# Kernel optimization log

Hardware: AMD Instinct MI355X
Metric: run time of the kernel (lower is better)

## Reference

```python
import jax, jax.numpy as jnp
import numpy as np

SEQ, D_IN, D_OUT = 8192, 768, 128


def setup_inputs() -> dict:
    key = jax.random.key(0)
    k1, k2, k3, k4 = jax.random.split(key, 4)
    x = jax.random.normal(k1, (SEQ, D_IN), dtype=jnp.float32)
    # torch nn.Linear weights are stored as [d_out, d_in]
    scale = 1.0 / np.sqrt(D_IN)
    w_query = jax.random.normal(k2, (D_OUT, D_IN), dtype=jnp.float32) * scale
    w_key = jax.random.normal(k3, (D_OUT, D_IN), dtype=jnp.float32) * scale
    w_value = jax.random.normal(k4, (D_OUT, D_IN), dtype=jnp.float32) * scale
    return {"x": x, "w_query": w_query, "w_key": w_key, "w_value": w_value}


def reference(x, w_query, w_key, w_value):
    # Linear with bias=False: y = x @ W.T   (W is [d_out, d_in])
    q = x @ w_query.T                      # [N, d_out]
    k = x @ w_key.T                        # [N, d_out]
    v = x @ w_value.T                      # [N, d_out]
    inv_sqrt_d = 1.0 / jnp.sqrt(jnp.float32(k.shape[-1]))
    scores = (q @ k.T) * inv_sqrt_d        # [N, N] -- fully materialized, as in source
    weights = jax.nn.softmax(scores, axis=-1)
    return weights @ v                     # [N, d_out]
```

## Files before the change

### kernel.cpp

```cpp
#include <hip/hip_runtime.h>
#include <stdint.h>

#define SEQ 8192
#define DIN 768
#define DOUT 128

typedef __attribute__((ext_vector_type(8))) short short8;
typedef __attribute__((ext_vector_type(8))) unsigned short ushort8v;
typedef __attribute__((ext_vector_type(4))) float f32x4;

#define CEXPF (1.4426950408889634f * 0.08838834764831845f)

#if __has_builtin(__builtin_amdgcn_exp2f)
#define EXP2(x) __builtin_amdgcn_exp2f(x)
#else
#define EXP2(x) __builtin_exp2f(x)
#endif

__device__ __forceinline__ unsigned short f2bf(float f) {
  return (unsigned short)((__float_as_uint(f) + 0x8000u) >> 16);
}

__device__ __forceinline__ void gload_lds16(const void* g, void* l) {
  __builtin_amdgcn_global_load_lds(
      (const __attribute__((address_space(1))) void*)g,
      (__attribute__((address_space(3))) void*)l, 16, 0, 0);
}

__global__ void wconv_kernel(const float* __restrict__ wq,
                             const float* __restrict__ wk,
                             const float* __restrict__ wv,
                             unsigned short* __restrict__ Wb) {
  int idx4 = (blockIdx.x * 256 + threadIdx.x) * 4;
  int z = idx4 / (DOUT * DIN);
  int rem = idx4 - z * (DOUT * DIN);
  const float* src = (z == 0) ? wq : (z == 1) ? wk : wv;
  float4 v = *(const float4*)(src + rem);
  float sc = (z == 0) ? CEXPF : 1.0f;
  ushort4 o;
  o.x = f2bf(v.x * sc); o.y = f2bf(v.y * sc);
  o.z = f2bf(v.z * sc); o.w = f2bf(v.w * sc);
  *(ushort4*)(Wb + idx4) = o;
}

__launch_bounds__(256, 3)
__global__ void qkv_kernel(const float* __restrict__ x,
                           const unsigned short* __restrict__ Wb,
                           unsigned short* __restrict__ Qb,
                           unsigned short* __restrict__ Kb,
                           unsigned short* __restrict__ Vtb) {
  __shared__ unsigned short smem[4352];
  unsigned short* xs = smem;

  const int t    = threadIdx.x;
  const int w    = t >> 6;
  const int lane = t & 63;
  const int g    = lane >> 4;
  const int r    = lane & 15;
  const int z    = blockIdx.y;
  const int m0   = blockIdx.x * 32;
  const unsigned short* Wz = Wb + (size_t)z * DOUT * DIN;

  f32x4 acc[2][2];
#pragma unroll
  for (int i = 0; i < 2; i++)
#pragma unroll
    for (int j = 0; j < 2; j++) acc[i][j] = 0.f;

  const int srow = t >> 3;
  const int scol = (t & 7) * 4;

#pragma unroll 1
  for (int kb = 0; kb < DIN; kb += 32) {
    short8 af[2];
#pragma unroll
    for (int mt = 0; mt < 2; mt++)
      af[mt] = *(const short8*)(Wz + (size_t)(w * 32 + mt * 16 + r) * DIN + kb + g * 8);
    float4 xv = *(const float4*)(x + (size_t)(m0 + srow) * DIN + kb + scol);
    ushort4 xb;
    xb.x = f2bf(xv.x); xb.y = f2bf(xv.y); xb.z = f2bf(xv.z); xb.w = f2bf(xv.w);
    *(ushort4*)&xs[srow * 40 + scol] = xb;
    __syncthreads();
    short8 bf[2];
#pragma unroll
    for (int nt = 0; nt < 2; nt++)
      bf[nt] = *(const short8*)&xs[(nt * 16 + r) * 40 + g * 8];
#pragma unroll
    for (int mt = 0; mt < 2; mt++)
#pragma unroll
      for (int nt = 0; nt < 2; nt++)
        acc[mt][nt] = __builtin_amdgcn_mfma_f32_16x16x32_bf16(af[mt], bf[nt], acc[mt][nt], 0, 0, 0);
    __syncthreads();
  }

  if (z < 2) {
    unsigned short* out = (z == 0) ? Qb : Kb;
#pragma unroll
    for (int mt = 0; mt < 2; mt++)
#pragma unroll
      for (int nt = 0; nt < 2; nt++) {
        ushort4 o;
        o.x = f2bf(acc[mt][nt][0]); o.y = f2bf(acc[mt][nt][1]);
        o.z = f2bf(acc[mt][nt][2]); o.w = f2bf(acc[mt][nt][3]);
        *(ushort4*)(out + (size_t)(m0 + nt * 16 + r) * DOUT + w * 32 + mt * 16 + g * 4) = o;
      }
  } else {
    unsigned short* ct = smem;
#pragma unroll
    for (int mt = 0; mt < 2; mt++)
#pragma unroll
      for (int nt = 0; nt < 2; nt++) {
        ushort4 o;
        o.x = f2bf(acc[mt][nt][0]); o.y = f2bf(acc[mt][nt][1]);
        o.z = f2bf(acc[mt][nt][2]); o.w = f2bf(acc[mt][nt][3]);
        *(ushort4*)&ct[(nt * 16 + r) * 136 + w * 32 + mt * 16 + g * 4] = o;
      }
    __syncthreads();
    int col  = t >> 1;
    int half = (t & 1) * 16;
#pragma unroll
    for (int h2 = 0; h2 < 2; h2++) {
      ushort8v a;
#pragma unroll
      for (int i = 0; i < 8; i++) a[i] = ct[(half + h2 * 8 + i) * 136 + col];
      *(ushort8v*)(Vtb + (size_t)col * SEQ + m0 + half + h2 * 8) = a;
    }
  }
}

__launch_bounds__(256, 2)
__global__ void attn_kernel(const unsigned short* __restrict__ Qb,
                            const unsigned short* __restrict__ Kb,
                            const unsigned short* __restrict__ Vtb,
                            float* __restrict__ Opart,
                            float* __restrict__ lpart) {
  __shared__ unsigned char lds[51200];
  unsigned char* Kl = lds;
  unsigned char* Vl = lds + 16384;

  const int t    = threadIdx.x;
  const int wave = t >> 6;
  const int lane = t & 63;
  const int g    = lane >> 4;
  const int r    = lane & 15;
  unsigned short* Pl = (unsigned short*)(lds + 32768 + wave * 4608);

  const int qb = blockIdx.x;
  const int sp = blockIdx.y;
  const int q0 = qb * 128 + wave * 32;

  short8 qf[2][4];
#pragma unroll
  for (int nt = 0; nt < 2; nt++)
#pragma unroll
    for (int kc = 0; kc < 4; kc++)
      qf[nt][kc] = *(const short8*)(Qb + (size_t)(q0 + nt * 16 + r) * DOUT + kc * 32 + g * 8);

  short8 onesf;
#pragma unroll
  for (int j = 0; j < 8; j++) onesf[j] = (r == 0) ? (short)0x3F80 : (short)0;

  f32x4 oacc[2][8];
  f32x4 lacc[2];
#pragma unroll
  for (int st = 0; st < 2; st++) {
    lacc[st] = 0.f;
#pragma unroll
    for (int n = 0; n < 8; n++) oacc[st][n] = 0.f;
  }

#pragma unroll 1
  for (int it = 0; it < 16; it++) {
    const int kv0 = sp * 1024 + it * 64;
#pragma unroll
    for (int c = 0; c < 4; c++) {
      int idx = (wave * 4 + c) * 64 + lane;
      int krow = idx >> 4, kch = idx & 15;
      gload_lds16(Kb + ((size_t)(kv0 + krow) << 7) + ((kch ^ (krow & 15)) << 3),
                  Kl + ((wave * 4 + c) << 10) + (lane << 4));
      int d = idx >> 3, c2 = idx & 7;
      gload_lds16(Vtb + (size_t)d * SEQ + kv0 + ((c2 ^ (d & 7)) << 3),
                  Vl + ((wave * 4 + c) << 10) + (lane << 4));
    }
    __syncthreads();

    f32x4 sf[4][2];
#pragma unroll
    for (int mt = 0; mt < 4; mt++)
#pragma unroll
      for (int nt = 0; nt < 2; nt++) sf[mt][nt] = 0.f;
#pragma unroll
    for (int mt = 0; mt < 4; mt++) {
      int row = mt * 16 + r;
#pragma unroll
      for (int kc = 0; kc < 4; kc++) {
        short8 kf = *(const short8*)(Kl + row * 256 + (((kc * 4 + g) ^ (row & 15)) << 4));
        sf[mt][0] = __builtin_amdgcn_mfma_f32_16x16x32_bf16(kf, qf[0][kc], sf[mt][0], 0, 0, 0);
        sf[mt][1] = __builtin_amdgcn_mfma_f32_16x16x32_bf16(kf, qf[1][kc], sf[mt][1], 0, 0, 0);
      }
    }

#pragma unroll
    for (int mt = 0; mt < 4; mt++)
#pragma unroll
      for (int nt = 0; nt < 2; nt++) {
        ushort4 p;
        p.x = f2bf(EXP2(sf[mt][nt][0]));
        p.y = f2bf(EXP2(sf[mt][nt][1]));
        p.z = f2bf(EXP2(sf[mt][nt][2]));
        p.w = f2bf(EXP2(sf[mt][nt][3]));
        *(ushort4*)(Pl + (nt * 16 + r) * 72 + mt * 16 + g * 4) = p;
      }
    short8 pf[2][2];
#pragma unroll
    for (int st = 0; st < 2; st++)
#pragma unroll
      for (int c2 = 0; c2 < 2; c2++)
        pf[st][c2] = *(const short8*)(Pl + (st * 16 + r) * 72 + c2 * 32 + g * 8);

#pragma unroll
    for (int nt = 0; nt < 8; nt++) {
      int d = nt * 16 + r;
#pragma unroll
      for (int c2 = 0; c2 < 2; c2++) {
        short8 vf = *(const short8*)(Vl + d * 128 + (((c2 * 4 + g) ^ (d & 7)) << 4));
        oacc[0][nt] = __builtin_amdgcn_mfma_f32_16x16x32_bf16(pf[0][c2], vf, oacc[0][nt], 0, 0, 0);
        oacc[1][nt] = __builtin_amdgcn_mfma_f32_16x16x32_bf16(pf[1][c2], vf, oacc[1][nt], 0, 0, 0);
      }
    }
#pragma unroll
    for (int st = 0; st < 2; st++) {
      lacc[st] = __builtin_amdgcn_mfma_f32_16x16x32_bf16(pf[st][0], onesf, lacc[st], 0, 0, 0);
      lacc[st] = __builtin_amdgcn_mfma_f32_16x16x32_bf16(pf[st][1], onesf, lacc[st], 0, 0, 0);
    }
    __syncthreads();
  }

  const size_t pbase = (size_t)sp * SEQ;
#pragma unroll
  for (int st = 0; st < 2; st++)
#pragma unroll
    for (int rr = 0; rr < 4; rr++) {
      int qrow = q0 + st * 16 + g * 4 + rr;
#pragma unroll
      for (int nt = 0; nt < 8; nt++)
        Opart[(pbase + qrow) * DOUT + nt * 16 + r] = oacc[st][nt][rr];
      if (r == 0) lpart[pbase + qrow] = lacc[st][rr];
    }
}

__global__ void combine_kernel(const float* __restrict__ Opart,
                               const float* __restrict__ lpart,
                               float* __restrict__ out) {
  int idx = blockIdx.x * 256 + threadIdx.x;
  int s   = idx >> 5;
  int d4  = (idx & 31) * 4;
  float L = 0.f;
  f32x4 acc = 0.f;
#pragma unroll
  for (int p = 0; p < 8; p++) {
    L += lpart[p * SEQ + s];
    acc += *(const f32x4*)(Opart + ((size_t)p * SEQ + s) * DOUT + d4);
  }
  f32x4 res = acc * (1.0f / L);
  *(f32x4*)(out + (size_t)s * DOUT + d4) = res;
}

extern "C" void kernel_launch(void* const* d_in, const int* in_sizes, int n_in,
                              void* d_out, int out_size, void* d_ws, size_t ws_size,
                              hipStream_t stream) {
  const float* x  = (const float*)d_in[0];
  const float* wq = (const float*)d_in[1];
  const float* wk = (const float*)d_in[2];
  const float* wv = (const float*)d_in[3];
  float* out = (float*)d_out;

  unsigned short* Qb  = (unsigned short*)d_ws;
  unsigned short* Kb  = Qb + (size_t)SEQ * DOUT;
  unsigned short* Vtb = Kb + (size_t)SEQ * DOUT;
  float* Opart = (float*)(Vtb + (size_t)SEQ * DOUT);
  float* lpart = Opart + (size_t)8 * SEQ * DOUT;
  unsigned short* Wb  = (unsigned short*)Opart;
  if (ws_size < (size_t)(6291456 + 33554432 + 262144)) return;

  wconv_kernel<<<dim3(288), 256, 0, stream>>>(wq, wk, wv, Wb);
  qkv_kernel<<<dim3(256, 3), 256, 0, stream>>>(x, Wb, Qb, Kb, Vtb);
  attn_kernel<<<dim3(64, 8), 256, 0, stream>>>(Qb, Kb, Vtb, Opart, lpart);
  combine_kernel<<<dim3(1024), 256, 0, stream>>>(Opart, lpart, out);
}
```

Before: 136.4 us.

## Pre-convert x to bf16 and retile QKV projection with async LDS loads

The separate weight-conversion kernel now also converts x to bf16 up front. The QKV projection uses 128-row tiles with a K step of 64, and stages both x and W into XOR-swizzled LDS through global_load_lds. This is meant to raise data reuse per block and cut redundant global W reads in the projection stage. The cost is an extra full pass over x plus a bf16 copy in workspace, and only 192 blocks, which may underfill the GPU.

```diff
diff --git a/kernel.cpp b/kernel.cpp
--- a/kernel.cpp
+++ b/kernel.cpp
@@ -27,30 +27,45 @@
       (__attribute__((address_space(3))) void*)l, 16, 0, 0);
 }
 
-__global__ void wconv_kernel(const float* __restrict__ wq,
-                             const float* __restrict__ wk,
-                             const float* __restrict__ wv,
-                             unsigned short* __restrict__ Wb) {
+#define XELEMS (SEQ * DIN)
+#define WELEMS (DOUT * DIN)
+__global__ void conv_kernel(const float* __restrict__ x,
+                            const float* __restrict__ wq,
+                            const float* __restrict__ wk,
+                            const float* __restrict__ wv,
+                            unsigned short* __restrict__ xb,
+                            unsigned short* __restrict__ Wb) {
   int idx4 = (blockIdx.x * 256 + threadIdx.x) * 4;
-  int z = idx4 / (DOUT * DIN);
-  int rem = idx4 - z * (DOUT * DIN);
-  const float* src = (z == 0) ? wq : (z == 1) ? wk : wv;
-  float4 v = *(const float4*)(src + rem);
-  float sc = (z == 0) ? CEXPF : 1.0f;
+  const float* src;
+  unsigned short* dst;
+  float sc = 1.0f;
+  if (idx4 < XELEMS) {
+    src = x + idx4;
+    dst = xb + idx4;
+  } else {
+    int wi = idx4 - XELEMS;
+    int z  = wi / WELEMS;
+    int rem = wi - z * WELEMS;
+    src = ((z == 0) ? wq : (z == 1) ? wk : wv) + rem;
+    dst = Wb + wi;
+    if (z == 0) sc = CEXPF;
+  }
+  float4 v = *(const float4*)src;
   ushort4 o;
   o.x = f2bf(v.x * sc); o.y = f2bf(v.y * sc);
   o.z = f2bf(v.z * sc); o.w = f2bf(v.w * sc);
-  *(ushort4*)(Wb + idx4) = o;
-}
-
-__launch_bounds__(256, 3)
-__global__ void qkv_kernel(const float* __restrict__ x,
+  *(ushort4*)dst = o;
+}
+
+__launch_bounds__(256, 2)
+__global__ void qkv_kernel(const unsigned short* __restrict__ xb,
                            const unsigned short* __restrict__ Wb,
                            unsigned short* __restrict__ Qb,
                            unsigned short* __restrict__ Kb,
                            unsigned short* __restrict__ Vtb) {
-  __shared__ unsigned short smem[4352];
-  unsigned short* xs = smem;
+  __shared__ unsigned char lds_u[35072];
+  unsigned char* xs = lds_u;
+  unsigned char* ws = lds_u + 16384;
 
   const int t    = threadIdx.x;
   const int w    = t >> 6;
@@ -58,38 +73,49 @@
   const int g    = lane >> 4;
   const int r    = lane & 15;
   const int z    = blockIdx.y;
-  const int m0   = blockIdx.x * 32;
-  const unsigned short* Wz = Wb + (size_t)z * DOUT * DIN;
-
-  f32x4 acc[2][2];
+  const int m0   = blockIdx.x * 128;
+  const unsigned short* Wz = Wb + (size_t)z * WELEMS;
+
+  f32x4 acc[2][8];
 #pragma unroll
   for (int i = 0; i < 2; i++)
 #pragma unroll
-    for (int j = 0; j < 2; j++) acc[i][j] = 0.f;
-
-  const int srow = t >> 3;
-  const int scol = (t & 7) * 4;
+    for (int j = 0; j < 8; j++) acc[i][j] = 0.f;
 
 #pragma unroll 1
-  for (int kb = 0; kb < DIN; kb += 32) {
-    short8 af[2];
+  for (int kb = 0; kb < DIN; kb += 64) {
+#pragma unroll
+    for (int c = 0; c < 4; c++) {
+      int ci = (w * 4 + c) * 64 + lane;
+      int row = ci >> 3, ch = ci & 7;
+      int sch = ch ^ (row & 7);
+      gload_lds16(xb + (size_t)(m0 + row) * DIN + kb + sch * 8,
+                  xs + ((w * 4 + c) << 10) + (lane << 4));
+      gload_lds16(Wz + (size_t)row * DIN + kb + sch * 8,
+                  ws + ((w * 4 + c) << 10) + (lane << 4));
+    }
+    __syncthreads();
+
+    short8 af[2][2], bf[2];
 #pragma unroll
     for (int mt = 0; mt < 2; mt++)
-      af[mt] = *(const short8*)(Wz + (size_t)(w * 32 + mt * 16 + r) * DIN + kb + g * 8);
-    float4 xv = *(const float4*)(x + (size_t)(m0 + srow) * DIN + kb + scol);
-    ushort4 xb;
-    xb.x = f2bf(xv.x); xb.y = f2bf(xv.y); xb.z = f2bf(xv.z); xb.w = f2bf(xv.w);
-    *(ushort4*)&xs[srow * 40 + scol] = xb;
-    __syncthreads();
-    short8 bf[2];
-#pragma unroll
-    for (int nt = 0; nt < 2; nt++)
-      bf[nt] = *(const short8*)&xs[(nt * 16 + r) * 40 + g * 8];
-#pragma unroll
-    for (int mt = 0; mt < 2; mt++)
-#pragma unroll
-      for (int nt = 0; nt < 2; nt++)
-        acc[mt][nt] = __builtin_amdgcn_mfma_f32_16x16x32_bf16(af[mt], bf[nt], acc[mt][nt], 0, 0, 0);
+#pragma unroll
+      for (int kc = 0; kc < 2; kc++) {
+        int row = w * 32 + mt * 16 + r;
+        af[mt][kc] = *(const short8*)(ws + row * 128 + (((kc * 4 + g) ^ (r & 7)) << 4));
+      }
+#pragma unroll
+    for (int nt = 0; nt < 8; nt++) {
+      int row = nt * 16 + r;
+#pragma unroll
+      for (int kc = 0; kc < 2; kc++)
+        bf[kc] = *(const short8*)(xs + row * 128 + (((kc * 4 + g) ^ (r & 7)) << 4));
+#pragma unroll
+      for (int mt = 0; mt < 2; mt++) {
+        acc[mt][nt] = __builtin_amdgcn_mfma_f32_16x16x32_bf16(af[mt][0], bf[0], acc[mt][nt], 0, 0, 0);
+        acc[mt][nt] = __builtin_amdgcn_mfma_f32_16x16x32_bf16(af[mt][1], bf[1], acc[mt][nt], 0, 0, 0);
+      }
+    }
     __syncthreads();
   }
 
@@ -98,18 +124,18 @@
 #pragma unroll
     for (int mt = 0; mt < 2; mt++)
 #pragma unroll
-      for (int nt = 0; nt < 2; nt++) {
+      for (int nt = 0; nt < 8; nt++) {
         ushort4 o;
         o.x = f2bf(acc[mt][nt][0]); o.y = f2bf(acc[mt][nt][1]);
         o.z = f2bf(acc[mt][nt][2]); o.w = f2bf(acc[mt][nt][3]);
         *(ushort4*)(out + (size_t)(m0 + nt * 16 + r) * DOUT + w * 32 + mt * 16 + g * 4) = o;
       }
   } else {
-    unsigned short* ct = smem;
+    unsigned short* ct = (unsigned short*)lds_u;
 #pragma unroll
     for (int mt = 0; mt < 2; mt++)
 #pragma unroll
-      for (int nt = 0; nt < 2; nt++) {
+      for (int nt = 0; nt < 8; nt++) {
         ushort4 o;
         o.x = f2bf(acc[mt][nt][0]); o.y = f2bf(acc[mt][nt][1]);
         o.z = f2bf(acc[mt][nt][2]); o.w = f2bf(acc[mt][nt][3]);
@@ -117,13 +143,13 @@
       }
     __syncthreads();
     int col  = t >> 1;
-    int half = (t & 1) * 16;
-#pragma unroll
-    for (int h2 = 0; h2 < 2; h2++) {
+    int half = (t & 1) * 64;
+#pragma unroll
+    for (int h = 0; h < 8; h++) {
       ushort8v a;
 #pragma unroll
-      for (int i = 0; i < 8; i++) a[i] = ct[(half + h2 * 8 + i) * 136 + col];
-      *(ushort8v*)(Vtb + (size_t)col * SEQ + m0 + half + h2 * 8) = a;
+      for (int i = 0; i < 8; i++) a[i] = ct[(half + h * 8 + i) * 136 + col];
+      *(ushort8v*)(Vtb + (size_t)col * SEQ + m0 + half + h * 8) = a;
     }
   }
 }
@@ -280,11 +306,12 @@
   unsigned short* Vtb = Kb + (size_t)SEQ * DOUT;
   float* Opart = (float*)(Vtb + (size_t)SEQ * DOUT);
   float* lpart = Opart + (size_t)8 * SEQ * DOUT;
-  unsigned short* Wb  = (unsigned short*)Opart;
+  unsigned short* xb = (unsigned short*)Opart;
+  unsigned short* Wb = xb + (size_t)XELEMS;
   if (ws_size < (size_t)(6291456 + 33554432 + 262144)) return;
 
-  wconv_kernel<<<dim3(288), 256, 0, stream>>>(wq, wk, wv, Wb);
-  qkv_kernel<<<dim3(256, 3), 256, 0, stream>>>(x, Wb, Qb, Kb, Vtb);
+  conv_kernel<<<dim3(6432), 256, 0, stream>>>(x, wq, wk, wv, xb, Wb);
+  qkv_kernel<<<dim3(64, 3), 256, 0, stream>>>(xb, Wb, Qb, Kb, Vtb);
   attn_kernel<<<dim3(64, 8), 256, 0, stream>>>(Qb, Kb, Vtb, Opart, lpart);
   combine_kernel<<<dim3(1024), 256, 0, stream>>>(Opart, lpart, out);
 }
```

After: 136.9 us. About the same (+0.3%).
